# Kernel optimization log

Hardware: AMD Instinct MI355X
Metric: run time of the kernel (lower is better)

## Reference

```python
import jax, jax.numpy as jnp
import numpy as np

GROUP_SIZE = 128  # infeatures // n_groups = 4096 // 32


def setup_inputs() -> dict:
    key = jax.random.key(0)
    k1, k2, k3, k4 = jax.random.split(key, 4)
    M, K, N = 256, 4096, 4096
    n_groups = K // GROUP_SIZE  # 32
    A = jax.random.normal(k1, (M, K), dtype=jnp.float32)
    # uint4 quantized weights, stored unpacked as int32 in [0, 16)
    qweight = jax.random.randint(k2, (N, K), 0, 16, dtype=jnp.int32)
    scales = jax.random.uniform(k3, (N, n_groups), dtype=jnp.float32) * 0.05 + 1e-3
    zeros = jax.random.uniform(k4, (N, n_groups), dtype=jnp.float32) * 15.0
    return {"A": A, "qweight": qweight, "scales": scales, "zeros": zeros}


def reference(A, qweight, scales, zeros):
    # Fused dequant + GEMM: W[n,k] = (q[n,k] - zeros[n, k//G]) * scales[n, k//G]
    N, K = qweight.shape
    s = jnp.repeat(scales, GROUP_SIZE, axis=1)   # [N, K]
    z = jnp.repeat(zeros, GROUP_SIZE, axis=1)    # [N, K]
    W = (qweight.astype(A.dtype) - z) * s        # dequantized weight [N, K]
    # Linear: Y = A @ W^T  -> [M, N]
    return jnp.einsum('mk,nk->mn', A, W)
```

## Files before the change

### kernel.cpp

```cpp
#include <hip/hip_runtime.h>

typedef __attribute__((ext_vector_type(8))) short bf16x8;
typedef __attribute__((ext_vector_type(4))) float f32x4;

#define MDIM 256
#define NDIM 4096
#define KDIM 4096
#define NGRP 32
#define BM 128
#define BN 32
#define BK 64
#define SPLITK 2
#define KLOC (KDIM / SPLITK)
#define NTL (KLOC / BK)

typedef const __attribute__((address_space(1))) void* gas_ptr;
typedef __attribute__((address_space(3))) void* las_ptr;

__device__ __forceinline__ unsigned short f2bf(float f) {
  union { float f; unsigned int u; } v;
  v.f = f;
  unsigned int r = v.u + 0x7FFFu + ((v.u >> 16) & 1u);
  return (unsigned short)(r >> 16);
}

__device__ __forceinline__ void gl_lds16(const void* g, void* l) {
  __builtin_amdgcn_global_load_lds((gas_ptr)g, (las_ptr)l, 16, 0, 0);
}

__global__ void convA_kernel(const float* __restrict__ A,
                             unsigned short* __restrict__ Ab) {
  int i = blockIdx.x * 256 + threadIdx.x;
  float4 v = reinterpret_cast<const float4*>(A)[i];
  ushort4 o;
  o.x = f2bf(v.x); o.y = f2bf(v.y); o.z = f2bf(v.z); o.w = f2bf(v.w);
  reinterpret_cast<ushort4*>(Ab)[i] = o;
}

__global__ __launch_bounds__(256, 2) void gemm_kernel(
    const unsigned short* __restrict__ Ab, const int* __restrict__ qw,
    const float* __restrict__ sc, const float* __restrict__ zr,
    float* __restrict__ out) {
  __shared__ __align__(16) unsigned short A_lds[4][BM * BK];
  __shared__ __align__(16) unsigned short W_lds[2][BN * BK];
  __shared__ float s_lds[BN * 16];
  __shared__ float zs_lds[BN * 16];

  const int tid = threadIdx.x;
  const int lane = tid & 63;
  const int wave = tid >> 6;
  const int wm = wave >> 1;
  const int wn = wave & 1;

  const int bid = blockIdx.x;
  const int x = bid & 7;
  const int j = bid >> 3;
  const int r = x * 16 + (j >> 2);
  const int c = j & 3;
  const int m0 = (c & 1) * BM;
  const int ks = c >> 1;
  const int n0 = r * BN;

  for (int i = tid; i < BN * 16; i += 256) {
    int n = i >> 4;
    int g16 = i & 15;
    float s = sc[(size_t)(n0 + n) * NGRP + ks * 16 + g16];
    float z = zr[(size_t)(n0 + n) * NGRP + ks * 16 + g16];
    s_lds[i] = s;
    zs_lds[i] = z * s;
  }

  const unsigned short* Abase = Ab + (size_t)m0 * KDIM + ks * KLOC;
  const int wrow = tid >> 3;
  const int wc = tid & 7;
  const int* qbase = qw + (size_t)(n0 + wrow) * KDIM + ks * KLOC + wc * 8;

  int4 qr[4][2];

  auto loadW = [&](int t, int idx) {
    const int* p = qbase + t * BK;
    qr[idx][0] = *reinterpret_cast<const int4*>(p);
    qr[idx][1] = *reinterpret_cast<const int4*>(p + 4);
  };
  auto stageA = [&](int t, int b) {
#pragma unroll
    for (int i = 0; i < 4; ++i) {
      int cid = i * 256 + tid;
      int row = cid >> 3;
      int cp = cid & 7;
      int cs = cp ^ (row & 7);
      const unsigned short* g = Abase + (size_t)row * KDIM + t * BK + cs * 8;
      gl_lds16(g, &A_lds[b][(i * 256 + wave * 64) * 8]);
    }
  };
  auto writeW = [&](int t, int b, int idx) {
    int gg = t >> 1;
    float s = s_lds[wrow * 16 + gg];
    float zs = zs_lds[wrow * 16 + gg];
    int q[8] = {qr[idx][0].x, qr[idx][0].y, qr[idx][0].z, qr[idx][0].w,
                qr[idx][1].x, qr[idx][1].y, qr[idx][1].z, qr[idx][1].w};
    bf16x8 w;
#pragma unroll
    for (int jj = 0; jj < 8; ++jj)
      w[jj] = (short)f2bf(fmaf((float)q[jj], s, -zs));
    *reinterpret_cast<bf16x8*>(
        &W_lds[b][wrow * BK + ((wc ^ (wrow & 7)) << 3)]) = w;
  };

  f32x4 acc[4];
#pragma unroll
  for (int i = 0; i < 4; ++i) acc[i] = (f32x4){0.f, 0.f, 0.f, 0.f};

  const int l15 = lane & 15;
  const int lhi = lane >> 4;
  const int ar0 = wm * 64 + l15;
  const int asw = ar0 & 7;
  const int br = wn * 16 + l15;
  const int bsw = br & 7;

  auto compute = [&](int ab, int wb) {
#pragma unroll
    for (int kss = 0; kss < 2; ++kss) {
      bf16x8 bfr = *reinterpret_cast<const bf16x8*>(
          &W_lds[wb][br * BK + ((((kss << 2) + lhi) ^ bsw) << 3)]);
#pragma unroll
      for (int mi = 0; mi < 4; ++mi) {
        bf16x8 afr = *reinterpret_cast<const bf16x8*>(
            &A_lds[ab][(ar0 + mi * 16) * BK + ((((kss << 2) + lhi) ^ asw) << 3)]);
        acc[mi] = __builtin_amdgcn_mfma_f32_16x16x32_bf16(afr, bfr, acc[mi], 0, 0, 0);
      }
    }
  };

  loadW(0, 0); stageA(0, 0);
  loadW(1, 1); stageA(1, 1);
  loadW(2, 2); stageA(2, 2);

  asm volatile("s_waitcnt lgkmcnt(0)" ::: "memory");
  __builtin_amdgcn_s_barrier();
  __builtin_amdgcn_sched_barrier(0);
  writeW(0, 0, 0);
  asm volatile("s_waitcnt vmcnt(12) lgkmcnt(0)" ::: "memory");
  __builtin_amdgcn_s_barrier();
  __builtin_amdgcn_sched_barrier(0);

  for (int tb = 0; tb < NTL; tb += 4) {
#pragma unroll
    for (int u = 0; u < 4; ++u) {
      const int t = tb + u;
      const int tp = (t + 3 < NTL) ? (t + 3) : 0;
      loadW(tp, (u + 3) & 3);
      stageA(tp, (u + 3) & 3);
      compute(u, u & 1);
      if (t + 1 < NTL) writeW(t + 1, (u + 1) & 1, (u + 1) & 3);
      asm volatile("s_waitcnt vmcnt(12) lgkmcnt(0)" ::: "memory");
      __builtin_amdgcn_s_barrier();
      __builtin_amdgcn_sched_barrier(0);
    }
  }

  const int col = n0 + wn * 16 + l15;
  const int rb = m0 + wm * 64 + (lhi << 2);
#pragma unroll
  for (int mi = 0; mi < 4; ++mi)
#pragma unroll
    for (int jj = 0; jj < 4; ++jj)
      unsafeAtomicAdd(&out[(size_t)(rb + mi * 16 + jj) * NDIM + col],
                      acc[mi][jj]);
}

extern "C" void kernel_launch(void* const* d_in, const int* in_sizes, int n_in,
                              void* d_out, int out_size, void* d_ws, size_t ws_size,
                              hipStream_t stream) {
  const float* A = (const float*)d_in[0];
  const int* qw = (const int*)d_in[1];
  const float* sc = (const float*)d_in[2];
  const float* zr = (const float*)d_in[3];
  float* out = (float*)d_out;
  unsigned short* Ab = (unsigned short*)d_ws;

  hipMemsetAsync(d_out, 0, (size_t)MDIM * NDIM * sizeof(float), stream);
  convA_kernel<<<(MDIM * KDIM / 4) / 256, 256, 0, stream>>>(A, Ab);
  gemm_kernel<<<(MDIM / BM) * (NDIM / BN) * SPLITK, 256, 0, stream>>>(
      Ab, qw, sc, zr, out);
}
```

Measured before the change: 136.9 us.

## Pack int4 weights into nibbles in a fused prep kernel before GEMM

```diff
diff --git a/kernel.cpp b/kernel.cpp
--- a/kernel.cpp
+++ b/kernel.cpp
@@ -6,6 +6,7 @@
 #define MDIM 256
 #define NDIM 4096
 #define KDIM 4096
+#define KP8 (KDIM / 8)
 #define NGRP 32
 #define BM 128
 #define BN 32
@@ -28,6 +29,27 @@
   __builtin_amdgcn_global_load_lds((gas_ptr)g, (las_ptr)l, 16, 0, 0);
 }
 
+__global__ void prep_kernel(const float* __restrict__ A, const int* __restrict__ q,
+                            unsigned short* __restrict__ Ab,
+                            unsigned int* __restrict__ qp) {
+  int i = blockIdx.x * 256 + threadIdx.x;
+  if (i < NDIM * KP8) {
+    const int4* p = reinterpret_cast<const int4*>(q) + (size_t)i * 2;
+    int4 a = p[0], b = p[1];
+    unsigned int d = (unsigned)(a.x & 15) | ((unsigned)(a.y & 15) << 4) |
+                     ((unsigned)(a.z & 15) << 8) | ((unsigned)(a.w & 15) << 12) |
+                     ((unsigned)(b.x & 15) << 16) | ((unsigned)(b.y & 15) << 20) |
+                     ((unsigned)(b.z & 15) << 24) | ((unsigned)(b.w & 15) << 28);
+    qp[i] = d;
+  } else {
+    int j = i - NDIM * KP8;
+    float4 v = reinterpret_cast<const float4*>(A)[j];
+    ushort4 o;
+    o.x = f2bf(v.x); o.y = f2bf(v.y); o.z = f2bf(v.z); o.w = f2bf(v.w);
+    reinterpret_cast<ushort4*>(Ab)[j] = o;
+  }
+}
+
 __global__ void convA_kernel(const float* __restrict__ A,
                              unsigned short* __restrict__ Ab) {
   int i = blockIdx.x * 256 + threadIdx.x;
@@ -37,7 +59,135 @@
   reinterpret_cast<ushort4*>(Ab)[i] = o;
 }
 
-__global__ __launch_bounds__(256, 2) void gemm_kernel(
+__global__ __launch_bounds__(256, 2) void gemm_pk(
+    const unsigned short* __restrict__ Ab, const unsigned int* __restrict__ qp,
+    const float* __restrict__ sc, const float* __restrict__ zr,
+    float* __restrict__ out) {
+  __shared__ __align__(16) unsigned short A_lds[4][BM * BK];
+  __shared__ __align__(16) unsigned short W_lds[2][BN * BK];
+  __shared__ float s_lds[BN * 16];
+  __shared__ float zs_lds[BN * 16];
+
+  const int tid = threadIdx.x;
+  const int lane = tid & 63;
+  const int wave = tid >> 6;
+  const int wm = wave >> 1;
+  const int wn = wave & 1;
+
+  const int bid = blockIdx.x;
+  const int x = bid & 7;
+  const int j = bid >> 3;
+  const int r = x * 16 + (j >> 2);
+  const int c = j & 3;
+  const int m0 = (c & 1) * BM;
+  const int ks = c >> 1;
+  const int n0 = r * BN;
+
+  for (int i = tid; i < BN * 16; i += 256) {
+    int n = i >> 4;
+    int g16 = i & 15;
+    float s = sc[(size_t)(n0 + n) * NGRP + ks * 16 + g16];
+    float z = zr[(size_t)(n0 + n) * NGRP + ks * 16 + g16];
+    s_lds[i] = s;
+    zs_lds[i] = z * s;
+  }
+
+  const unsigned short* Abase = Ab + (size_t)m0 * KDIM + ks * KLOC;
+  const int wrow = tid >> 3;
+  const int wc = tid & 7;
+  const unsigned int* qpbase =
+      qp + (size_t)(n0 + wrow) * KP8 + ks * (KLOC / 8) + wc;
+
+  unsigned int qd[4];
+
+  auto loadW = [&](int t, int idx) { qd[idx] = qpbase[t * 8]; };
+  auto stageA = [&](int t, int b) {
+#pragma unroll
+    for (int i = 0; i < 4; ++i) {
+      int cid = i * 256 + tid;
+      int row = cid >> 3;
+      int cp = cid & 7;
+      int cs = cp ^ (row & 7);
+      const unsigned short* g = Abase + (size_t)row * KDIM + t * BK + cs * 8;
+      gl_lds16(g, &A_lds[b][(i * 256 + wave * 64) * 8]);
+    }
+  };
+  auto writeW = [&](int t, int b, int idx) {
+    int gg = t >> 1;
+    float s = s_lds[wrow * 16 + gg];
+    float zs = zs_lds[wrow * 16 + gg];
+    unsigned int d = qd[idx];
+    bf16x8 w;
+#pragma unroll
+    for (int jj = 0; jj < 8; ++jj)
+      w[jj] = (short)f2bf(fmaf((float)((d >> (4 * jj)) & 15u), s, -zs));
+    *reinterpret_cast<bf16x8*>(
+        &W_lds[b][wrow * BK + ((wc ^ (wrow & 7)) << 3)]) = w;
+  };
+
+  f32x4 acc[4];
+#pragma unroll
+  for (int i = 0; i < 4; ++i) acc[i] = (f32x4){0.f, 0.f, 0.f, 0.f};
+
+  const int l15 = lane & 15;
+  const int lhi = lane >> 4;
+  const int ar0 = wm * 64 + l15;
+  const int asw = ar0 & 7;
+  const int br = wn * 16 + l15;
+  const int bsw = br & 7;
+
+  auto compute = [&](int ab, int wb) {
+#pragma unroll
+    for (int kss = 0; kss < 2; ++kss) {
+      bf16x8 bfr = *reinterpret_cast<const bf16x8*>(
+          &W_lds[wb][br * BK + ((((kss << 2) + lhi) ^ bsw) << 3)]);
+#pragma unroll
+      for (int mi = 0; mi < 4; ++mi) {
+        bf16x8 afr = *reinterpret_cast<const bf16x8*>(
+            &A_lds[ab][(ar0 + mi * 16) * BK + ((((kss << 2) + lhi) ^ asw) << 3)]);
+        acc[mi] = __builtin_amdgcn_mfma_f32_16x16x32_bf16(afr, bfr, acc[mi], 0, 0, 0);
+      }
+    }
+  };
+
+  loadW(0, 0); stageA(0, 0);
+  loadW(1, 1); stageA(1, 1);
+  loadW(2, 2); stageA(2, 2);
+
+  asm volatile("s_waitcnt lgkmcnt(0)" ::: "memory");
+  __builtin_amdgcn_s_barrier();
+  __builtin_amdgcn_sched_barrier(0);
+  writeW(0, 0, 0);
+  asm volatile("s_waitcnt vmcnt(10) lgkmcnt(0)" ::: "memory");
+  __builtin_amdgcn_s_barrier();
+  __builtin_amdgcn_sched_barrier(0);
+
+  for (int tb = 0; tb < NTL; tb += 4) {
+#pragma unroll
+    for (int u = 0; u < 4; ++u) {
+      const int t = tb + u;
+      const int tp = (t + 3 < NTL) ? (t + 3) : 0;
+      loadW(tp, (u + 3) & 3);
+      stageA(tp, (u + 3) & 3);
+      compute(u, u & 1);
+      if (t + 1 < NTL) writeW(t + 1, (u + 1) & 1, (u + 1) & 3);
+      asm volatile("s_waitcnt vmcnt(10) lgkmcnt(0)" ::: "memory");
+      __builtin_amdgcn_s_barrier();
+      __builtin_amdgcn_sched_barrier(0);
+    }
+  }
+
+  const int col = n0 + wn * 16 + l15;
+  const int rb = m0 + wm * 64 + (lhi << 2);
+#pragma unroll
+  for (int mi = 0; mi < 4; ++mi)
+#pragma unroll
+    for (int jj = 0; jj < 4; ++jj)
+      unsafeAtomicAdd(&out[(size_t)(rb + mi * 16 + jj) * NDIM + col],
+                      acc[mi][jj]);
+}
+
+__global__ __launch_bounds__(256, 2) void gemm_r3(
     const unsigned short* __restrict__ Ab, const int* __restrict__ qw,
     const float* __restrict__ sc, const float* __restrict__ zr,
     float* __restrict__ out) {
@@ -177,10 +327,19 @@
   const float* sc = (const float*)d_in[2];
   const float* zr = (const float*)d_in[3];
   float* out = (float*)d_out;
-  unsigned short* Ab = (unsigned short*)d_ws;
 
   hipMemsetAsync(d_out, 0, (size_t)MDIM * NDIM * sizeof(float), stream);
-  convA_kernel<<<(MDIM * KDIM / 4) / 256, 256, 0, stream>>>(A, Ab);
-  gemm_kernel<<<(MDIM / BM) * (NDIM / BN) * SPLITK, 256, 0, stream>>>(
-      Ab, qw, sc, zr, out);
-}
+
+  if (ws_size >= (10u << 20)) {
+    unsigned short* Ab = (unsigned short*)d_ws;
+    unsigned int* qp = (unsigned int*)((char*)d_ws + (2u << 20));
+    prep_kernel<<<9216, 256, 0, stream>>>(A, qw, Ab, qp);
+    gemm_pk<<<(MDIM / BM) * (NDIM / BN) * SPLITK, 256, 0, stream>>>(
+        Ab, qp, sc, zr, out);
+  } else {
+    unsigned short* Ab = (unsigned short*)d_ws;
+    convA_kernel<<<(MDIM * KDIM / 4) / 256, 256, 0, stream>>>(A, Ab);
+    gemm_r3<<<(MDIM / BM) * (NDIM / BN) * SPLITK, 256, 0, stream>>>(
+        Ab, qw, sc, zr, out);
+  }
+}
```

Result: no change. 134.5 us (-1.8%).

## Enlarge GEMM tile to full M with 512-thread blocks and split-K of four

Applied to the files above, without the earlier changes.

```diff
diff --git a/kernel.cpp b/kernel.cpp
--- a/kernel.cpp
+++ b/kernel.cpp
@@ -7,12 +7,6 @@
 #define NDIM 4096
 #define KDIM 4096
 #define NGRP 32
-#define BM 128
-#define BN 32
-#define BK 64
-#define SPLITK 2
-#define KLOC (KDIM / SPLITK)
-#define NTL (KLOC / BK)
 
 typedef const __attribute__((address_space(1))) void* gas_ptr;
 typedef __attribute__((address_space(3))) void* las_ptr;
@@ -37,14 +31,22 @@
   reinterpret_cast<ushort4*>(Ab)[i] = o;
 }
 
-__global__ __launch_bounds__(256, 2) void gemm_kernel(
+#define BM 256
+#define BN 64
+#define BK 64
+#define SPLITK 4
+#define KLOC (KDIM / SPLITK)
+#define NTL (KLOC / BK)
+#define GPS (KLOC / 128)
+
+__global__ __launch_bounds__(512, 1) void gemm_raw(
     const unsigned short* __restrict__ Ab, const int* __restrict__ qw,
     const float* __restrict__ sc, const float* __restrict__ zr,
     float* __restrict__ out) {
   __shared__ __align__(16) unsigned short A_lds[4][BM * BK];
   __shared__ __align__(16) unsigned short W_lds[2][BN * BK];
-  __shared__ float s_lds[BN * 16];
-  __shared__ float zs_lds[BN * 16];
+  __shared__ float s_lds[BN * GPS];
+  __shared__ float zs_lds[BN * GPS];
 
   const int tid = threadIdx.x;
   const int lane = tid & 63;
@@ -53,27 +55,25 @@
   const int wn = wave & 1;
 
   const int bid = blockIdx.x;
-  const int x = bid & 7;
+  const int xcd = bid & 7;
   const int j = bid >> 3;
-  const int r = x * 16 + (j >> 2);
-  const int c = j & 3;
-  const int m0 = (c & 1) * BM;
-  const int ks = c >> 1;
-  const int n0 = r * BN;
+  const int ks = j >> 3;
+  const int nl = j & 7;
+  const int n0 = (xcd * 8 + nl) * BN;
+  const int kbase = ks * KLOC;
 
-  for (int i = tid; i < BN * 16; i += 256) {
-    int n = i >> 4;
-    int g16 = i & 15;
-    float s = sc[(size_t)(n0 + n) * NGRP + ks * 16 + g16];
-    float z = zr[(size_t)(n0 + n) * NGRP + ks * 16 + g16];
-    s_lds[i] = s;
-    zs_lds[i] = z * s;
+  {
+    int n = tid >> 3, g = tid & 7;
+    float s = sc[(size_t)(n0 + n) * NGRP + ks * GPS + g];
+    float z = zr[(size_t)(n0 + n) * NGRP + ks * GPS + g];
+    s_lds[tid] = s;
+    zs_lds[tid] = z * s;
   }
 
-  const unsigned short* Abase = Ab + (size_t)m0 * KDIM + ks * KLOC;
+  const unsigned short* Abase = Ab + kbase;
   const int wrow = tid >> 3;
   const int wc = tid & 7;
-  const int* qbase = qw + (size_t)(n0 + wrow) * KDIM + ks * KLOC + wc * 8;
+  const int* qbase = qw + (size_t)(n0 + wrow) * KDIM + kbase + wc * 8;
 
   int4 qr[4][2];
 
@@ -85,18 +85,18 @@
   auto stageA = [&](int t, int b) {
 #pragma unroll
     for (int i = 0; i < 4; ++i) {
-      int cid = i * 256 + tid;
+      int cid = i * 512 + tid;
       int row = cid >> 3;
       int cp = cid & 7;
       int cs = cp ^ (row & 7);
       const unsigned short* g = Abase + (size_t)row * KDIM + t * BK + cs * 8;
-      gl_lds16(g, &A_lds[b][(i * 256 + wave * 64) * 8]);
+      gl_lds16(g, &A_lds[b][(i * 512 + wave * 64) * 8]);
     }
   };
   auto writeW = [&](int t, int b, int idx) {
     int gg = t >> 1;
-    float s = s_lds[wrow * 16 + gg];
-    float zs = zs_lds[wrow * 16 + gg];
+    float s = s_lds[wrow * GPS + gg];
+    float zs = zs_lds[wrow * GPS + gg];
     int q[8] = {qr[idx][0].x, qr[idx][0].y, qr[idx][0].z, qr[idx][0].w,
                 qr[idx][1].x, qr[idx][1].y, qr[idx][1].z, qr[idx][1].w};
     bf16x8 w;
@@ -107,27 +107,33 @@
         &W_lds[b][wrow * BK + ((wc ^ (wrow & 7)) << 3)]) = w;
   };
 
-  f32x4 acc[4];
+  f32x4 acc[4][2];
 #pragma unroll
-  for (int i = 0; i < 4; ++i) acc[i] = (f32x4){0.f, 0.f, 0.f, 0.f};
+  for (int i = 0; i < 4; ++i)
+#pragma unroll
+    for (int n = 0; n < 2; ++n) acc[i][n] = (f32x4){0.f, 0.f, 0.f, 0.f};
 
   const int l15 = lane & 15;
   const int lhi = lane >> 4;
   const int ar0 = wm * 64 + l15;
   const int asw = ar0 & 7;
-  const int br = wn * 16 + l15;
-  const int bsw = br & 7;
 
   auto compute = [&](int ab, int wb) {
 #pragma unroll
     for (int kss = 0; kss < 2; ++kss) {
-      bf16x8 bfr = *reinterpret_cast<const bf16x8*>(
-          &W_lds[wb][br * BK + ((((kss << 2) + lhi) ^ bsw) << 3)]);
 #pragma unroll
-      for (int mi = 0; mi < 4; ++mi) {
-        bf16x8 afr = *reinterpret_cast<const bf16x8*>(
-            &A_lds[ab][(ar0 + mi * 16) * BK + ((((kss << 2) + lhi) ^ asw) << 3)]);
-        acc[mi] = __builtin_amdgcn_mfma_f32_16x16x32_bf16(afr, bfr, acc[mi], 0, 0, 0);
+      for (int ni = 0; ni < 2; ++ni) {
+        const int br = wn * 32 + ni * 16 + l15;
+        bf16x8 bfr = *reinterpret_cast<const bf16x8*>(
+            &W_lds[wb][br * BK + ((((kss << 2) + lhi) ^ (br & 7)) << 3)]);
+#pragma unroll
+        for (int mi = 0; mi < 4; ++mi) {
+          bf16x8 afr = *reinterpret_cast<const bf16x8*>(
+              &A_lds[ab][(ar0 + mi * 16) * BK +
+                         ((((kss << 2) + lhi) ^ asw) << 3)]);
+          acc[mi][ni] = __builtin_amdgcn_mfma_f32_16x16x32_bf16(
+              afr, bfr, acc[mi][ni], 0, 0, 0);
+        }
       }
     }
   };
@@ -159,14 +165,16 @@
     }
   }
 
-  const int col = n0 + wn * 16 + l15;
-  const int rb = m0 + wm * 64 + (lhi << 2);
+  const int col = n0 + wn * 32 + l15;
+  const int rb = wm * 64 + (lhi << 2);
 #pragma unroll
   for (int mi = 0; mi < 4; ++mi)
 #pragma unroll
-    for (int jj = 0; jj < 4; ++jj)
-      unsafeAtomicAdd(&out[(size_t)(rb + mi * 16 + jj) * NDIM + col],
-                      acc[mi][jj]);
+    for (int ni = 0; ni < 2; ++ni)
+#pragma unroll
+      for (int jj = 0; jj < 4; ++jj)
+        unsafeAtomicAdd(&out[(size_t)(rb + mi * 16 + jj) * NDIM + col + ni * 16],
+                        acc[mi][ni][jj]);
 }
 
 extern "C" void kernel_launch(void* const* d_in, const int* in_sizes, int n_in,
@@ -181,6 +189,5 @@
 
   hipMemsetAsync(d_out, 0, (size_t)MDIM * NDIM * sizeof(float), stream);
   convA_kernel<<<(MDIM * KDIM / 4) / 256, 256, 0, stream>>>(A, Ab);
-  gemm_kernel<<<(MDIM / BM) * (NDIM / BN) * SPLITK, 256, 0, stream>>>(
-      Ab, qw, sc, zr, out);
+  gemm_raw<<<(NDIM / BN) * SPLITK, 512, 0, stream>>>(Ab, qw, sc, zr, out);
 }
```

Measured after the change: 127.1 us. -7.2%, faster.
